# Performance work log

Hardware: AMD Instinct MI355X
Metric: run time of the kernel (lower is better)

## Reference

```python
import jax, jax.numpy as jnp
import numpy as np

N_EXAMPLES = 10  # hardcoded repeat_interleave(10) in the source

def setup_inputs() -> dict:
    key = jax.random.key(0)
    k1, k2, k3, k4 = jax.random.split(key, 4)
    B, L, S, H = 8, 256, 512, 1024
    return {
        "output": jax.random.normal(k1, (B * N_EXAMPLES, L, H), dtype=jnp.float32),
        "context0": jax.random.normal(k2, (B * N_EXAMPLES, L, H), dtype=jnp.float32),
        "context1": jax.random.normal(k3, (B, S, H), dtype=jnp.float32),
        "mask": jnp.zeros((B * N_EXAMPLES, L), dtype=bool),
        "W_out": jax.random.normal(k4, (H, 3 * H), dtype=jnp.float32) * 0.02,
        "b_out": jnp.zeros((H,), dtype=jnp.float32),
    }

def reference(output, context0, context1, mask, W_out, b_out):
    # output, context0: [B*10, L, H]; context1: [B, S, H]
    # NOTE: in the torch source, `attn.data.masked_fill(mask, -inf)` is NOT
    # in-place and its result is discarded, so the mask has no effect on the
    # math. We reproduce that faithfully: `mask` is unused.
    del mask
    set_ctx = jnp.repeat(context1, N_EXAMPLES, axis=0)  # [B*10, S, H]
    # example-attention branch: bmm -> softmax -> bmm
    ex_attn = jax.nn.softmax(jnp.einsum('bld,bsd->bls', output, context0), axis=-1)  # [B*10, L, L]
    # set-attention branch: bmm -> softmax -> bmm
    set_attn = jax.nn.softmax(jnp.einsum('bld,bsd->bls', output, set_ctx), axis=-1)  # [B*10, L, S]
    ex_c = jnp.einsum('bls,bsd->bld', ex_attn, context0)   # [B*10, L, H]
    set_c = jnp.einsum('bls,bsd->bld', set_attn, set_ctx)  # [B*10, L, H]
    all_info = jnp.concatenate([output, ex_c, set_c], axis=-1)  # [B*10, L, 3H]
    out = jnp.tanh(jnp.einsum('blk,hk->blh', all_info, W_out) + b_out)  # [B*10, L, H]
    return (out, ex_attn, set_attn)
```

## Files before the change

### kernel.cpp

```cpp
#include <hip/hip_runtime.h>
#include <stdint.h>
#include <math.h>

typedef unsigned short u16;
typedef __attribute__((ext_vector_type(8))) short short8;
typedef __attribute__((ext_vector_type(4))) float floatx4;

__device__ __forceinline__ u16 f32_to_bf16(float f) {
    union { float f; uint32_t u; } v; v.f = f;
    uint32_t r = v.u + 0x7FFF + ((v.u >> 16) & 1);
    return (u16)(r >> 16);
}
__device__ __forceinline__ float bf16_to_f32(u16 h) {
    union { uint32_t u; float f; } v; v.u = ((uint32_t)h) << 16; return v.f;
}

__device__ __forceinline__ void gl_lds16(const u16* g, u16* l) {
    __builtin_amdgcn_global_load_lds(
        (const __attribute__((address_space(1))) void*)g,
        (__attribute__((address_space(3))) void*)l, 16, 0, 0);
}


__global__ void split_kernel(const float4* __restrict__ x, ushort4* __restrict__ hi,
                             ushort4* __restrict__ lo, long n4) {
    long i = (long)blockIdx.x * blockDim.x + threadIdx.x;
    if (i >= n4) return;
    float4 v = x[i];
    ushort4 h, l;
    h.x = f32_to_bf16(v.x); l.x = f32_to_bf16(v.x - bf16_to_f32(h.x));
    h.y = f32_to_bf16(v.y); l.y = f32_to_bf16(v.y - bf16_to_f32(h.y));
    h.z = f32_to_bf16(v.z); l.z = f32_to_bf16(v.z - bf16_to_f32(h.z));
    h.w = f32_to_bf16(v.w); l.w = f32_to_bf16(v.w - bf16_to_f32(h.w));
    hi[i] = h; lo[i] = l;
}

__global__ void conv_kernel(const float4* __restrict__ x, ushort4* __restrict__ hi, long n4) {
    long i = (long)blockIdx.x * blockDim.x + threadIdx.x;
    if (i >= n4) return;
    float4 v = x[i];
    ushort4 h;
    h.x = f32_to_bf16(v.x); h.y = f32_to_bf16(v.y);
    h.z = f32_to_bf16(v.z); h.w = f32_to_bf16(v.w);
    hi[i] = h;
}

__global__ void transpose_u16(const u16* __restrict__ src, u16* __restrict__ dst,
                              int R, int C) {
    __shared__ u16 tile[32][34];
    long base = (long)blockIdx.z * R * C;
    int c0 = blockIdx.x * 32, r0 = blockIdx.y * 32;
    #pragma unroll
    for (int i = threadIdx.y; i < 32; i += 8)
        tile[i][threadIdx.x] = src[base + (long)(r0 + i) * C + c0 + threadIdx.x];
    __syncthreads();
    #pragma unroll
    for (int i = threadIdx.y; i < 32; i += 8)
        dst[base + (long)(c0 + i) * R + r0 + threadIdx.x] = tile[threadIdx.x][i];
}

template <int VPT>
__global__ void softmax_rows(float* __restrict__ data, u16* __restrict__ outb) {
    int row = blockIdx.x * 4 + (threadIdx.x >> 6);
    int lane = threadIdx.x & 63;
    long base = (long)row * (VPT * 64) + lane;
    float v[VPT];
    #pragma unroll
    for (int i = 0; i < VPT; ++i) v[i] = data[base + i * 64];
    float m = v[0];
    #pragma unroll
    for (int i = 1; i < VPT; ++i) m = fmaxf(m, v[i]);
    #pragma unroll
    for (int off = 32; off > 0; off >>= 1) m = fmaxf(m, __shfl_xor(m, off, 64));
    float s = 0.f;
    #pragma unroll
    for (int i = 0; i < VPT; ++i) { v[i] = __expf(v[i] - m); s += v[i]; }
    #pragma unroll
    for (int off = 32; off > 0; off >>= 1) s += __shfl_xor(s, off, 64);
    float inv = 1.0f / s;
    #pragma unroll
    for (int i = 0; i < VPT; ++i) {
        float r = v[i] * inv;
        data[base + i * 64] = r;
        outb[base + i * 64] = f32_to_bf16(r);
    }
}

struct GemmP {
    const u16* A[3];
    const u16* B[3];
    const u16* B2[3];
    long strideAb, strideBb, strideB2b, strideCb, strideC2b;
    int bdiv, bdiv2, nseg, Kper, kshift, kmask, nt, lda, ldb, ldb2, ldc, ldc2, mode;
    int gx, gy, nx1;
    float* Cf; float* Cf2; u16* Cb; const float* bias;
};

__global__ __launch_bounds__(512, 2) void gemm_bt8(GemmP p) {
    __shared__ u16 As[32768];
    __shared__ u16 Bs[32768];
    const int tid  = threadIdx.x;
    const int lane = tid & 63;
    const int wave = tid >> 6;
    const int quad = lane >> 4;
    const int l15  = lane & 15;
    const int wr   = wave >> 2;
    const int wc   = wave & 3;

    const int f  = blockIdx.x;
    const int Tx = gridDim.x >> 3;
    const int t  = (f & 7) * Tx + (f >> 3);
    const int n  = t % p.gx;
    const int r  = t / p.gx;
    const int m0 = (r % p.gy) * 256;
    const int bz = r / p.gy;

    const u16* Bsegs[3];
    int ldb, ldc, nn, bdv;
    long bstr, cstr;
    float* Cf;
    if (n < p.nx1) {
        Bsegs[0] = p.B[0]; Bsegs[1] = p.B[1]; Bsegs[2] = p.B[2];
        ldb = p.ldb; ldc = p.ldc; bstr = p.strideBb; cstr = p.strideCb;
        Cf = p.Cf; bdv = p.bdiv; nn = n;
    } else {
        Bsegs[0] = p.B2[0]; Bsegs[1] = p.B2[1]; Bsegs[2] = p.B2[2];
        ldb = p.ldb2; ldc = p.ldc2; bstr = p.strideB2b; cstr = p.strideC2b;
        Cf = p.Cf2; bdv = p.bdiv2; nn = n - p.nx1;
    }
    const int n0 = nn * 256;

    const long aoff = (long)bz * p.strideAb + (long)m0 * p.lda;
    const long boff = (long)(bz / bdv) * bstr + (long)n0 * ldb;

    const int srow = tid >> 2;
    const int sgc  = ((tid & 3) ^ ((srow >> 1) & 3)) * 8;

    const int rA = wr * 128 + l15;
    const u16* pA = As + rA * 32 + ((quad ^ ((rA >> 1) & 3)) * 8);
    const int rB = wc * 64 + l15;
    const u16* pB = Bs + rB * 32 + ((quad ^ ((rB >> 1) & 3)) * 8);

    const int nt = p.nt;

    auto stA = [&](int kt, int kk) {
        if (kt < nt) {
            const int seg = kt >> p.kshift;
            const u16* g = p.A[seg] + aoff + (long)srow * p.lda
                         + (((kt & p.kmask) << 6) + kk * 32 + sgc);
            u16* d = &As[((((kt & 1) << 1) | kk) << 13) + tid * 8];
            gl_lds16(g, d);
            gl_lds16(g + (long)128 * p.lda, d + 4096);
        }
    };
    auto stB = [&](int kt, int kk) {
        if (kt < nt) {
            const int seg = kt >> p.kshift;
            const u16* g = Bsegs[seg] + boff + (long)srow * ldb
                         + (((kt & p.kmask) << 6) + kk * 32 + sgc);
            u16* d = &Bs[((((kt & 1) << 1) | kk) << 13) + tid * 8];
            gl_lds16(g, d);
            gl_lds16(g + (long)128 * ldb, d + 4096);
        }
    };

    floatx4 acc[8][4];
    #pragma unroll
    for (int i = 0; i < 8; ++i)
        #pragma unroll
        for (int j = 0; j < 4; ++j)
            acc[i][j] = (floatx4){0.f, 0.f, 0.f, 0.f};

    stA(0, 0); stB(0, 0); stA(0, 1); stB(0, 1); stA(1, 0); stB(1, 0);
    asm volatile("s_waitcnt vmcnt(4)" ::: "memory");
    __builtin_amdgcn_s_barrier();

    short8 af[4], bf[4];

#define QPHASE(SO, MH, LOADB, STAGE)                                        \
    {                                                                       \
        _Pragma("unroll")                                                   \
        for (int mi = 0; mi < 4; ++mi)                                      \
            af[mi] = *(const short8*)(pA + (SO) + (MH) * 2048 + mi * 512);  \
        if (LOADB) {                                                        \
            _Pragma("unroll")                                               \
            for (int ni = 0; ni < 4; ++ni)                                  \
                bf[ni] = *(const short8*)(pB + (SO) + ni * 512);            \
        }                                                                   \
        STAGE;                                                              \
        __builtin_amdgcn_s_barrier();                                       \
        asm volatile("s_waitcnt lgkmcnt(0)" ::: "memory");                  \
        __builtin_amdgcn_sched_barrier(0);                                  \
        __builtin_amdgcn_s_setprio(1);                                      \
        _Pragma("unroll")                                                   \
        for (int mi = 0; mi < 4; ++mi)                                      \
            _Pragma("unroll")                                               \
            for (int ni = 0; ni < 4; ++ni)                                  \
                acc[(MH) * 4 + mi][ni] =                                    \
                    __builtin_amdgcn_mfma_f32_16x16x32_bf16(                \
                        af[mi], bf[ni], acc[(MH) * 4 + mi][ni], 0, 0, 0);   \
        __builtin_amdgcn_s_setprio(0);                                      \
        __builtin_amdgcn_sched_barrier(0);                                  \
    }

    for (int kt = 0; kt < nt; ++kt) {
        const int so0 = (kt & 1) << 14;
        const int so1 = so0 + 8192;
        QPHASE(so0, 0, true,  stA(kt + 1, 1));
        __builtin_amdgcn_s_barrier();
        QPHASE(so0, 1, false, stB(kt + 1, 1));
        __builtin_amdgcn_s_barrier();
        QPHASE(so1, 0, true,  stA(kt + 2, 0));
        __builtin_amdgcn_s_barrier();
        QPHASE(so1, 1, false, stB(kt + 2, 0));
        if (kt + 2 < nt) {
            asm volatile("s_waitcnt vmcnt(4)" ::: "memory");
        } else {
            asm volatile("s_waitcnt vmcnt(0)" ::: "memory");
        }
        __builtin_amdgcn_s_barrier();
    }
#undef QPHASE

    const long coff = (long)bz * cstr;
    const int rb = m0 + wr * 128 + quad * 4;
    const int cb = n0 + wc * 64 + l15;
    if (p.mode == 2) {
        #pragma unroll
        for (int ni = 0; ni < 4; ++ni) {
            const float bv = p.bias[cb + ni * 16];
            #pragma unroll
            for (int mi = 0; mi < 8; ++mi)
                #pragma unroll
                for (int j = 0; j < 4; ++j)
                    Cf[coff + (long)(rb + mi * 16 + j) * ldc + cb + ni * 16] =
                        tanhf(acc[mi][ni][j] + bv);
        }
    } else if (p.mode == 0) {
        #pragma unroll
        for (int ni = 0; ni < 4; ++ni)
            #pragma unroll
            for (int mi = 0; mi < 8; ++mi)
                #pragma unroll
                for (int j = 0; j < 4; ++j)
                    Cf[coff + (long)(rb + mi * 16 + j) * ldc + cb + ni * 16] =
                        acc[mi][ni][j];
    } else {
        #pragma unroll
        for (int ni = 0; ni < 4; ++ni)
            #pragma unroll
            for (int mi = 0; mi < 8; ++mi)
                #pragma unroll
                for (int j = 0; j < 4; ++j)
                    p.Cb[coff + (long)(rb + mi * 16 + j) * ldc + cb + ni * 16] =
                        f32_to_bf16(acc[mi][ni][j]);
    }
}

__global__ __launch_bounds__(256) void gemm_bt(GemmP p) {
    __shared__ u16 As[128 * 64];
    __shared__ u16 Bs[128 * 64];
    const int tid  = threadIdx.x;
    const int lane = tid & 63;
    const int wave = tid >> 6;
    const int quad = lane >> 4;
    const int l15  = lane & 15;
    const int wm = (wave & 1) * 64;
    const int wn = (wave >> 1) * 64;

    const int f  = blockIdx.x;
    const int Tx = gridDim.x >> 3;
    const int t  = (f & 7) * Tx + (f >> 3);
    const int n  = t % p.gx;
    const int r  = t / p.gx;
    const int m0 = (r % p.gy) * 128;
    const int bz = r / p.gy;

    const u16* Bsegs[3];
    int ldb, ldc, nn, bdv;
    long bstr, cstr;
    float* Cf;
    if (n < p.nx1) {
        Bsegs[0] = p.B[0]; Bsegs[1] = p.B[1]; Bsegs[2] = p.B[2];
        ldb = p.ldb; ldc = p.ldc; bstr = p.strideBb; cstr = p.strideCb;
        Cf = p.Cf; bdv = p.bdiv; nn = n;
    } else {
        Bsegs[0] = p.B2[0]; Bsegs[1] = p.B2[1]; Bsegs[2] = p.B2[2];
        ldb = p.ldb2; ldc = p.ldc2; bstr = p.strideB2b; cstr = p.strideC2b;
        Cf = p.Cf2; bdv = p.bdiv2; nn = n - p.nx1;
    }
    const int n0 = nn * 128;

    const int stg_r8 = tid >> 3;
    const int stg_c  = ((tid & 7) ^ (stg_r8 & 7)) * 8;
    const int xorl   = l15 & 7;

    floatx4 acc[4][4];
    #pragma unroll
    for (int i = 0; i < 4; ++i)
        #pragma unroll
        for (int j = 0; j < 4; ++j)
            acc[i][j] = (floatx4){0.f, 0.f, 0.f, 0.f};

    const long aoff = (long)bz * p.strideAb + (long)m0 * p.lda;
    const long boff = (long)(bz / bdv) * bstr + (long)n0 * ldb;

    for (int seg = 0; seg < p.nseg; ++seg) {
        const u16* Ag = p.A[seg] + aoff;
        const u16* Bg = Bsegs[seg] + boff;
        for (int k0 = 0; k0 < p.Kper; k0 += 64) {
            __syncthreads();
            #pragma unroll
            for (int i = 0; i < 4; ++i) {
                const int rr = i * 32 + stg_r8;
                gl_lds16(Ag + (long)rr * p.lda + k0 + stg_c, &As[(i * 256 + tid) * 8]);
            }
            #pragma unroll
            for (int i = 0; i < 4; ++i) {
                const int rr = i * 32 + stg_r8;
                gl_lds16(Bg + (long)rr * ldb + k0 + stg_c, &Bs[(i * 256 + tid) * 8]);
            }
            __syncthreads();
            #pragma unroll
            for (int kk = 0; kk < 2; ++kk) {
                const int cs = ((kk * 4 + quad) ^ xorl) * 8;
                short8 af[4], bfr[4];
                #pragma unroll
                for (int i = 0; i < 4; ++i)
                    af[i] = *(const short8*)&As[(wm + i * 16 + l15) * 64 + cs];
                #pragma unroll
                for (int i = 0; i < 4; ++i)
                    bfr[i] = *(const short8*)&Bs[(wn + i * 16 + l15) * 64 + cs];
                #pragma unroll
                for (int mi = 0; mi < 4; ++mi)
                    #pragma unroll
                    for (int ni = 0; ni < 4; ++ni)
                        acc[mi][ni] = __builtin_amdgcn_mfma_f32_16x16x32_bf16(
                            af[mi], bfr[ni], acc[mi][ni], 0, 0, 0);
            }
        }
    }

    const long coff = (long)bz * cstr;
    const int rb = m0 + wm + quad * 4;
    const int cbase = n0 + wn + l15;
    if (p.mode == 2) {
        #pragma unroll
        for (int ni = 0; ni < 4; ++ni) {
            const float bv = p.bias[cbase + ni * 16];
            #pragma unroll
            for (int mi = 0; mi < 4; ++mi)
                #pragma unroll
                for (int j = 0; j < 4; ++j)
                    Cf[coff + (long)(rb + mi * 16 + j) * ldc + cbase + ni * 16] =
                        tanhf(acc[mi][ni][j] + bv);
        }
    } else if (p.mode == 0) {
        #pragma unroll
        for (int ni = 0; ni < 4; ++ni)
            #pragma unroll
            for (int mi = 0; mi < 4; ++mi)
                #pragma unroll
                for (int j = 0; j < 4; ++j)
                    Cf[coff + (long)(rb + mi * 16 + j) * ldc + cbase + ni * 16] =
                        acc[mi][ni][j];
    } else {
        #pragma unroll
        for (int ni = 0; ni < 4; ++ni)
            #pragma unroll
            for (int mi = 0; mi < 4; ++mi)
                #pragma unroll
                for (int j = 0; j < 4; ++j)
                    p.Cb[coff + (long)(rb + mi * 16 + j) * ldc + cbase + ni * 16] =
                        f32_to_bf16(acc[mi][ni][j]);
    }
}

extern "C" void kernel_launch(void* const* d_in, const int* in_sizes, int n_in,
                              void* d_out, int out_size, void* d_ws, size_t ws_size,
                              hipStream_t stream) {
    const int BT = 80, L = 256, S = 512, H = 1024;
    const long NO    = (long)BT * L * H;
    const long NC1   = (long)8 * S * H;
    const long NW    = (long)H * 3 * H;
    const long NEXA  = (long)BT * L * L;
    const long NSETA = (long)BT * L * S;

    const float* X    = (const float*)d_in[0];
    const float* C0   = (const float*)d_in[1];
    const float* C1   = (const float*)d_in[2];
    const float* Wf   = (const float*)d_in[4];
    const float* bias = (const float*)d_in[5];

    float* out  = (float*)d_out;
    float* exa  = out + NO;
    float* seta = exa + NEXA;

    char* wsb = (char*)d_ws;
    size_t off = 0;
    auto alloc = [&](long nbytes) -> void* {
        void* p = (void*)(wsb + off);
        off += ((size_t)nbytes + 255) & ~(size_t)255;
        return p;
    };
    u16* Xhi  = (u16*)alloc(NO * 2);
    u16* Xlo  = (u16*)alloc(NO * 2);
    u16* C0hi = (u16*)alloc(NO * 2);
    u16* C0lo = (u16*)alloc(NO * 2);
    u16* C1hi = (u16*)alloc(NC1 * 2);
    u16* C1lo = (u16*)alloc(NC1 * 2);
    u16* Wb   = (u16*)alloc(NW * 2);
    u16* exab = (u16*)alloc(NEXA * 2);
    u16* setab= (u16*)alloc(NSETA * 2);
    u16* C0T = C0lo;
    u16* C1T = C1lo;
    u16* exc = Xlo;
    u16* setc = C0hi;

    split_kernel<<<(int)(NO / 4 / 256), 256, 0, stream>>>((const float4*)X, (ushort4*)Xhi, (ushort4*)Xlo, NO / 4);
    split_kernel<<<(int)(NO / 4 / 256), 256, 0, stream>>>((const float4*)C0, (ushort4*)C0hi, (ushort4*)C0lo, NO / 4);
    split_kernel<<<(int)(NC1 / 4 / 256), 256, 0, stream>>>((const float4*)C1, (ushort4*)C1hi, (ushort4*)C1lo, NC1 / 4);
    conv_kernel<<<(int)(NW / 4 / 256), 256, 0, stream>>>((const float4*)Wf, (ushort4*)Wb, NW / 4);

    {
        GemmP p{};
        p.A[0] = Xhi;  p.A[1] = Xlo;  p.A[2] = Xhi;
        p.B[0]  = C0hi; p.B[1]  = C0hi; p.B[2]  = C0lo;
        p.B2[0] = C1hi; p.B2[1] = C1hi; p.B2[2] = C1lo;
        p.strideAb = (long)L * H;
        p.strideBb = (long)L * H;  p.strideB2b = (long)S * H;
        p.strideCb = (long)L * L;  p.strideC2b = (long)L * S;
        p.bdiv = 1; p.bdiv2 = 10;
        p.kshift = 4; p.kmask = 15; p.nt = 48;
        p.lda = H; p.ldb = H; p.ldb2 = H;
        p.ldc = L; p.ldc2 = S; p.mode = 0;
        p.gx = 3; p.gy = 1; p.nx1 = 1;
        p.Cf = exa; p.Cf2 = seta;
        gemm_bt8<<<dim3(3 * 1 * BT, 1, 1), 512, 0, stream>>>(p);
    }
    softmax_rows<4><<<BT * L / 4, 256, 0, stream>>>(exa, exab);
    softmax_rows<8><<<BT * L / 4, 256, 0, stream>>>(seta, setab);

    transpose_u16<<<dim3(H / 32, L / 32, BT), dim3(32, 8), 0, stream>>>(C0hi, C0T, L, H);
    transpose_u16<<<dim3(H / 32, S / 32, 8), dim3(32, 8), 0, stream>>>(C1hi, C1T, S, H);

    {
        GemmP p{};
        p.A[0] = exab; p.B[0] = C0T;
        p.strideAb = (long)L * L; p.strideBb = (long)H * L; p.strideCb = (long)L * H;
        p.bdiv = 1; p.kshift = 2; p.kmask = 3; p.nt = 4;
        p.lda = L; p.ldb = L; p.ldc = H; p.mode = 1;
        p.gx = 4; p.gy = 1; p.nx1 = 4;
        p.Cb = exc;
        gemm_bt8<<<dim3(4 * 1 * BT, 1, 1), 512, 0, stream>>>(p);
    }
    {
        GemmP p{};
        p.A[0] = setab; p.B[0] = C1T;
        p.strideAb = (long)L * S; p.strideBb = (long)H * S; p.strideCb = (long)L * H;
        p.bdiv = 10; p.kshift = 3; p.kmask = 7; p.nt = 8;
        p.lda = S; p.ldb = S; p.ldc = H; p.mode = 1;
        p.gx = 4; p.gy = 1; p.nx1 = 4;
        p.Cb = setc;
        gemm_bt8<<<dim3(4 * 1 * BT, 1, 1), 512, 0, stream>>>(p);
    }
    {
        GemmP p{};
        p.A[0] = Xhi; p.A[1] = exc; p.A[2] = setc;
        p.B[0] = Wb;  p.B[1] = Wb + 1024; p.B[2] = Wb + 2048;
        p.strideAb = 0; p.strideBb = 0; p.strideCb = 0;
        p.bdiv = 1; p.nseg = 3; p.Kper = H; p.lda = H; p.ldb = 3 * H; p.ldc = H; p.mode = 2;
        p.gx = 8; p.gy = BT * L / 128; p.nx1 = 8;
        p.Cf = out; p.bias = bias;
        gemm_bt<<<dim3(8 * (BT * L / 128), 1, 1), 256, 0, stream>>>(p);
    }
}
```

Before: 747.4 us.

## Triple-buffer output GEMM pipeline and fuse prep and softmax launches

```diff
diff --git a/kernel.cpp b/kernel.cpp
--- a/kernel.cpp
+++ b/kernel.cpp
@@ -22,27 +22,41 @@
 }
 
 
-__global__ void split_kernel(const float4* __restrict__ x, ushort4* __restrict__ hi,
-                             ushort4* __restrict__ lo, long n4) {
-    long i = (long)blockIdx.x * blockDim.x + threadIdx.x;
-    if (i >= n4) return;
-    float4 v = x[i];
-    ushort4 h, l;
+__device__ __forceinline__ void split4(const float4& v, ushort4& h, ushort4& l) {
     h.x = f32_to_bf16(v.x); l.x = f32_to_bf16(v.x - bf16_to_f32(h.x));
     h.y = f32_to_bf16(v.y); l.y = f32_to_bf16(v.y - bf16_to_f32(h.y));
     h.z = f32_to_bf16(v.z); l.z = f32_to_bf16(v.z - bf16_to_f32(h.z));
     h.w = f32_to_bf16(v.w); l.w = f32_to_bf16(v.w - bf16_to_f32(h.w));
-    hi[i] = h; lo[i] = l;
-}
-
-__global__ void conv_kernel(const float4* __restrict__ x, ushort4* __restrict__ hi, long n4) {
+}
+
+__global__ void prep_kernel(const float4* __restrict__ X, ushort4* __restrict__ Xhi,
+                            ushort4* __restrict__ Xlo,
+                            const float4* __restrict__ C0, ushort4* __restrict__ C0hi,
+                            ushort4* __restrict__ C0lo,
+                            const float4* __restrict__ C1, ushort4* __restrict__ C1hi,
+                            ushort4* __restrict__ C1lo,
+                            const float4* __restrict__ W, ushort4* __restrict__ Wb,
+                            long n4X, long n4C1, long n4W) {
     long i = (long)blockIdx.x * blockDim.x + threadIdx.x;
-    if (i >= n4) return;
-    float4 v = x[i];
-    ushort4 h;
-    h.x = f32_to_bf16(v.x); h.y = f32_to_bf16(v.y);
-    h.z = f32_to_bf16(v.z); h.w = f32_to_bf16(v.w);
-    hi[i] = h;
+    if (i < n4X) {
+        ushort4 h, l; split4(X[i], h, l); Xhi[i] = h; Xlo[i] = l; return;
+    }
+    i -= n4X;
+    if (i < n4X) {
+        ushort4 h, l; split4(C0[i], h, l); C0hi[i] = h; C0lo[i] = l; return;
+    }
+    i -= n4X;
+    if (i < n4C1) {
+        ushort4 h, l; split4(C1[i], h, l); C1hi[i] = h; C1lo[i] = l; return;
+    }
+    i -= n4C1;
+    if (i < n4W) {
+        float4 v = W[i];
+        ushort4 h;
+        h.x = f32_to_bf16(v.x); h.y = f32_to_bf16(v.y);
+        h.z = f32_to_bf16(v.z); h.w = f32_to_bf16(v.w);
+        Wb[i] = h;
+    }
 }
 
 __global__ void transpose_u16(const u16* __restrict__ src, u16* __restrict__ dst,
@@ -60,8 +74,9 @@
 }
 
 template <int VPT>
-__global__ void softmax_rows(float* __restrict__ data, u16* __restrict__ outb) {
-    int row = blockIdx.x * 4 + (threadIdx.x >> 6);
+__device__ __forceinline__ void softmax_body(float* __restrict__ data,
+                                             u16* __restrict__ outb, int blk) {
+    int row = blk * 4 + (threadIdx.x >> 6);
     int lane = threadIdx.x & 63;
     long base = (long)row * (VPT * 64) + lane;
     float v[VPT];
@@ -84,6 +99,14 @@
         data[base + i * 64] = r;
         outb[base + i * 64] = f32_to_bf16(r);
     }
+}
+
+__global__ void softmax_both(float* __restrict__ exa, u16* __restrict__ exab,
+                             float* __restrict__ seta, u16* __restrict__ setab,
+                             int nex) {
+    int b = blockIdx.x;
+    if (b < nex) softmax_body<4>(exa, exab, b);
+    else         softmax_body<8>(seta, setab, b - nex);
 }
 
 struct GemmP {
@@ -257,9 +280,9 @@
     }
 }
 
-__global__ __launch_bounds__(256) void gemm_bt(GemmP p) {
-    __shared__ u16 As[128 * 64];
-    __shared__ u16 Bs[128 * 64];
+__global__ __launch_bounds__(256) void gemm_bt3(GemmP p) {
+    __shared__ u16 As[3 * 4096];
+    __shared__ u16 Bs[3 * 4096];
     const int tid  = threadIdx.x;
     const int lane = tid & 63;
     const int wave = tid >> 6;
@@ -291,9 +314,39 @@
     }
     const int n0 = nn * 128;
 
-    const int stg_r8 = tid >> 3;
-    const int stg_c  = ((tid & 7) ^ (stg_r8 & 7)) * 8;
-    const int xorl   = l15 & 7;
+    const long aoff = (long)bz * p.strideAb + (long)m0 * p.lda;
+    const long boff = (long)(bz / bdv) * bstr + (long)n0 * ldb;
+
+    const int srow = tid >> 2;
+    const int sgc  = ((tid & 3) ^ ((srow >> 1) & 3)) * 8;
+
+    const int rA = wm + l15;
+    const int xA = (quad ^ ((rA >> 1) & 3)) * 8;
+    const int rB = wn + l15;
+    const int xB = (quad ^ ((rB >> 1) & 3)) * 8;
+
+    const int nt = p.nt;
+
+    auto stA = [&](int kt) {
+        if (kt < nt) {
+            const int seg = kt >> p.kshift;
+            const u16* g = p.A[seg] + aoff + (long)srow * p.lda
+                         + (((kt & p.kmask) << 5) + sgc);
+            u16* d = &As[(kt % 3) * 4096 + tid * 8];
+            gl_lds16(g, d);
+            gl_lds16(g + (long)64 * p.lda, d + 2048);
+        }
+    };
+    auto stB = [&](int kt) {
+        if (kt < nt) {
+            const int seg = kt >> p.kshift;
+            const u16* g = Bsegs[seg] + boff + (long)srow * ldb
+                         + (((kt & p.kmask) << 5) + sgc);
+            u16* d = &Bs[(kt % 3) * 4096 + tid * 8];
+            gl_lds16(g, d);
+            gl_lds16(g + (long)64 * ldb, d + 2048);
+        }
+    };
 
     floatx4 acc[4][4];
     #pragma unroll
@@ -302,43 +355,37 @@
         for (int j = 0; j < 4; ++j)
             acc[i][j] = (floatx4){0.f, 0.f, 0.f, 0.f};
 
-    const long aoff = (long)bz * p.strideAb + (long)m0 * p.lda;
-    const long boff = (long)(bz / bdv) * bstr + (long)n0 * ldb;
-
-    for (int seg = 0; seg < p.nseg; ++seg) {
-        const u16* Ag = p.A[seg] + aoff;
-        const u16* Bg = Bsegs[seg] + boff;
-        for (int k0 = 0; k0 < p.Kper; k0 += 64) {
-            __syncthreads();
-            #pragma unroll
-            for (int i = 0; i < 4; ++i) {
-                const int rr = i * 32 + stg_r8;
-                gl_lds16(Ag + (long)rr * p.lda + k0 + stg_c, &As[(i * 256 + tid) * 8]);
-            }
-            #pragma unroll
-            for (int i = 0; i < 4; ++i) {
-                const int rr = i * 32 + stg_r8;
-                gl_lds16(Bg + (long)rr * ldb + k0 + stg_c, &Bs[(i * 256 + tid) * 8]);
-            }
-            __syncthreads();
-            #pragma unroll
-            for (int kk = 0; kk < 2; ++kk) {
-                const int cs = ((kk * 4 + quad) ^ xorl) * 8;
-                short8 af[4], bfr[4];
-                #pragma unroll
-                for (int i = 0; i < 4; ++i)
-                    af[i] = *(const short8*)&As[(wm + i * 16 + l15) * 64 + cs];
-                #pragma unroll
-                for (int i = 0; i < 4; ++i)
-                    bfr[i] = *(const short8*)&Bs[(wn + i * 16 + l15) * 64 + cs];
-                #pragma unroll
-                for (int mi = 0; mi < 4; ++mi)
-                    #pragma unroll
-                    for (int ni = 0; ni < 4; ++ni)
-                        acc[mi][ni] = __builtin_amdgcn_mfma_f32_16x16x32_bf16(
-                            af[mi], bfr[ni], acc[mi][ni], 0, 0, 0);
-            }
-        }
+    stA(0); stB(0); stA(1); stB(1);
+    asm volatile("s_waitcnt vmcnt(4)" ::: "memory");
+    __builtin_amdgcn_s_barrier();
+
+    for (int kt = 0; kt < nt; ++kt) {
+        stA(kt + 2); stB(kt + 2);
+        const int so = (kt % 3) * 4096;
+        short8 af[4], bfr[4];
+        #pragma unroll
+        for (int i = 0; i < 4; ++i)
+            af[i] = *(const short8*)&As[so + (rA + i * 16) * 32 + xA];
+        #pragma unroll
+        for (int i = 0; i < 4; ++i)
+            bfr[i] = *(const short8*)&Bs[so + (rB + i * 16) * 32 + xB];
+        asm volatile("s_waitcnt lgkmcnt(0)" ::: "memory");
+        __builtin_amdgcn_sched_barrier(0);
+        __builtin_amdgcn_s_setprio(1);
+        #pragma unroll
+        for (int mi = 0; mi < 4; ++mi)
+            #pragma unroll
+            for (int ni = 0; ni < 4; ++ni)
+                acc[mi][ni] = __builtin_amdgcn_mfma_f32_16x16x32_bf16(
+                    af[mi], bfr[ni], acc[mi][ni], 0, 0, 0);
+        __builtin_amdgcn_s_setprio(0);
+        __builtin_amdgcn_sched_barrier(0);
+        if (kt + 2 < nt) {
+            asm volatile("s_waitcnt vmcnt(4)" ::: "memory");
+        } else {
+            asm volatile("s_waitcnt vmcnt(0)" ::: "memory");
+        }
+        __builtin_amdgcn_s_barrier();
     }
 
     const long coff = (long)bz * cstr;
@@ -417,10 +464,15 @@
     u16* exc = Xlo;
     u16* setc = C0hi;
 
-    split_kernel<<<(int)(NO / 4 / 256), 256, 0, stream>>>((const float4*)X, (ushort4*)Xhi, (ushort4*)Xlo, NO / 4);
-    split_kernel<<<(int)(NO / 4 / 256), 256, 0, stream>>>((const float4*)C0, (ushort4*)C0hi, (ushort4*)C0lo, NO / 4);
-    split_kernel<<<(int)(NC1 / 4 / 256), 256, 0, stream>>>((const float4*)C1, (ushort4*)C1hi, (ushort4*)C1lo, NC1 / 4);
-    conv_kernel<<<(int)(NW / 4 / 256), 256, 0, stream>>>((const float4*)Wf, (ushort4*)Wb, NW / 4);
+    {
+        const long n4X = NO / 4, n4C1 = NC1 / 4, n4W = NW / 4;
+        const long tot = 2 * n4X + n4C1 + n4W;
+        prep_kernel<<<(int)(tot / 256), 256, 0, stream>>>(
+            (const float4*)X, (ushort4*)Xhi, (ushort4*)Xlo,
+            (const float4*)C0, (ushort4*)C0hi, (ushort4*)C0lo,
+            (const float4*)C1, (ushort4*)C1hi, (ushort4*)C1lo,
+            (const float4*)Wf, (ushort4*)Wb, n4X, n4C1, n4W);
+    }
 
     {
         GemmP p{};
@@ -438,8 +490,7 @@
         p.Cf = exa; p.Cf2 = seta;
         gemm_bt8<<<dim3(3 * 1 * BT, 1, 1), 512, 0, stream>>>(p);
     }
-    softmax_rows<4><<<BT * L / 4, 256, 0, stream>>>(exa, exab);
-    softmax_rows<8><<<BT * L / 4, 256, 0, stream>>>(seta, setab);
+    softmax_both<<<2 * (BT * L / 4), 256, 0, stream>>>(exa, exab, seta, setab, BT * L / 4);
 
     transpose_u16<<<dim3(H / 32, L / 32, BT), dim3(32, 8), 0, stream>>>(C0hi, C0T, L, H);
     transpose_u16<<<dim3(H / 32, S / 32, 8), dim3(32, 8), 0, stream>>>(C1hi, C1T, S, H);
@@ -469,9 +520,10 @@
         p.A[0] = Xhi; p.A[1] = exc; p.A[2] = setc;
         p.B[0] = Wb;  p.B[1] = Wb + 1024; p.B[2] = Wb + 2048;
         p.strideAb = 0; p.strideBb = 0; p.strideCb = 0;
-        p.bdiv = 1; p.nseg = 3; p.Kper = H; p.lda = H; p.ldb = 3 * H; p.ldc = H; p.mode = 2;
+        p.bdiv = 1; p.kshift = 5; p.kmask = 31; p.nt = 96;
+        p.lda = H; p.ldb = 3 * H; p.ldc = H; p.mode = 2;
         p.gx = 8; p.gy = BT * L / 128; p.nx1 = 8;
         p.Cf = out; p.bias = bias;
-        gemm_bt<<<dim3(8 * (BT * L / 128), 1, 1), 256, 0, stream>>>(p);
-    }
-}
+        gemm_bt3<<<dim3(8 * (BT * L / 128), 1, 1), 256, 0, stream>>>(p);
+    }
+}
```

New measurement: 788.9 us. 5.6% more time.
